# Kernel optimization log

Hardware: AMD Instinct MI355X
Metric: run time of the kernel (lower is better)

## Reference

```python
import jax, jax.numpy as jnp
import numpy as np

B, C, L = 4, 256, 4096
H = 8
DK = C // H


def setup_inputs() -> dict:
    key = jax.random.key(0)
    kx, kq, kk, kv, kl = jax.random.split(key, 5)
    scale = 1.0 / np.sqrt(C)
    return {
        "x": jax.random.normal(kx, (B, C, L), dtype=jnp.float32),
        "Wq": jax.random.normal(kq, (C, C), dtype=jnp.float32) * scale,
        "Wk": jax.random.normal(kk, (C, C), dtype=jnp.float32) * scale,
        "Wv": jax.random.normal(kv, (C, C), dtype=jnp.float32) * scale,
        "Wl": jax.random.normal(kl, (C, C), dtype=jnp.float32) * scale,
    }


def reference(x, Wq, Wk, Wv, Wl):
    # Conv1d with kernel_size=1, no bias == channel-mixing matmul per position.
    def proj(W, t):  # W: [C_out, C_in], t: [B, C_in, L] -> [B, L, H, DK]
        y = jnp.einsum('oc,bcl->blo', W, t)
        return y.reshape(B, L, H, DK)

    q = proj(Wq, x)  # [B, L, H, DK]
    k = proj(Wk, x)
    v = proj(Wv, x)

    # scores: [B, H, L, L]
    scores = jnp.einsum('bqhd,bkhd->bhqk', q, k) / jnp.sqrt(jnp.float32(DK))
    p_attn = jax.nn.softmax(scores, axis=-1)
    # attention output with post-ReLU: [B, L, H, DK] -> [B, L, C]
    out = jax.nn.relu(jnp.einsum('bhqk,bkhd->bqhd', p_attn, v)).reshape(B, L, C)
    # last_conv: [B, C_out, L]
    return jnp.einsum('oc,blc->bol', Wl, out)
```

## Files before the change

kernel.cpp:

```cpp
#include <hip/hip_runtime.h>

#define L_DIM 4096
#define C_DIM 256
#define B_DIM 4
#define NH 8
#define DK 32

#define QSCALE 0.25507694f

typedef __bf16 bf16x8 __attribute__((ext_vector_type(8)));
typedef float  f32x4  __attribute__((ext_vector_type(4)));
typedef float  f32x8  __attribute__((ext_vector_type(8)));
typedef float  f32x16 __attribute__((ext_vector_type(16)));

static __device__ __forceinline__ unsigned pk_bf16(float lo, float hi) {
    unsigned a = __builtin_bit_cast(unsigned, lo) + 0x8000u;
    unsigned b = __builtin_bit_cast(unsigned, hi) + 0x8000u;
    return __builtin_amdgcn_perm(b, a, 0x07060302u);
}

__global__ __launch_bounds__(256) void transpose_x_kernel(
    const float* __restrict__ x, __bf16* __restrict__ xt)
{
    const int t  = threadIdx.x;
    const int l0 = blockIdx.x * 64;
    const int c0 = blockIdx.y * 64;
    const int b  = blockIdx.z;

    __shared__ __attribute__((aligned(16))) float T[64][65];

    {
        const int r  = t >> 2;
        const int lc = (t & 3) * 16;
        const float* xp = x + ((size_t)b * C_DIM + c0 + r) * L_DIM + l0 + lc;
        #pragma unroll
        for (int k = 0; k < 4; ++k)
            *(f32x4*)&T[r][lc + k * 4] = *(const f32x4*)(xp + k * 4);
    }
    __syncthreads();
    {
        const int l  = t >> 2;
        const int cc = (t & 3) * 16;
        unsigned u[8];
        #pragma unroll
        for (int i = 0; i < 8; ++i)
            u[i] = pk_bf16(T[cc + 2 * i][l], T[cc + 2 * i + 1][l]);
        __bf16* op = xt + ((size_t)b * L_DIM + l0 + l) * C_DIM + c0 + cc;
        *(uint4*)op       = make_uint4(u[0], u[1], u[2], u[3]);
        *(uint4*)(op + 8) = make_uint4(u[4], u[5], u[6], u[7]);
    }
}

__global__ __launch_bounds__(256) void proj_mfma_kernel(
    const __bf16* __restrict__ xt, const float* __restrict__ Wq,
    const float* __restrict__ Wk, const float* __restrict__ Wv,
    __bf16* __restrict__ Qb, __bf16* __restrict__ Kb, __bf16* __restrict__ Vb)
{
    const int t    = threadIdx.x;
    const int wave = t >> 6;
    const int lane = t & 63;
    const int n32  = lane & 31;
    const int hl   = lane >> 5;
    const int l0   = blockIdx.x * 128;
    const int ob   = blockIdx.y & 1;
    const int p    = blockIdx.y >> 1;
    const int b    = blockIdx.z;
    const float* W = (p == 0) ? Wq : ((p == 1) ? Wk : Wv);
    const float sc = (p == 0) ? QSCALE : 1.0f;

    __shared__ __attribute__((aligned(16))) __bf16 Wt[128][72];
    __shared__ __attribute__((aligned(16))) __bf16 Xs[128][72];

    const int wo  = t >> 1, wcc = (t & 1) * 32;
    const int xl  = t >> 1, xcc = (t & 1) * 32;
    const float*  wg = W + (size_t)(ob * 128 + wo) * C_DIM + wcc;
    const __bf16* xg = xt + ((size_t)b * L_DIM + l0 + xl) * C_DIM + xcc;

    const int moff = (wave & 1) * 64;
    const int noff = (wave >> 1) * 64;

    f32x16 acc[2][2];
    #pragma unroll
    for (int i = 0; i < 2; ++i)
        #pragma unroll
        for (int j = 0; j < 2; ++j)
            #pragma unroll
            for (int r = 0; r < 16; ++r) acc[i][j][r] = 0.f;

    unsigned wpk[16];
    bf16x8   xpr[4];
    #pragma unroll
    for (int k = 0; k < 8; ++k) {
        f32x4 wv = *(const f32x4*)(wg + k * 4);
        wpk[k * 2]     = pk_bf16(wv[0] * sc, wv[1] * sc);
        wpk[k * 2 + 1] = pk_bf16(wv[2] * sc, wv[3] * sc);
    }
    #pragma unroll
    for (int g = 0; g < 4; ++g) xpr[g] = *(const bf16x8*)(xg + g * 8);

    for (int bk = 0; bk < 4; ++bk) {
        __syncthreads();
        #pragma unroll
        for (int g = 0; g < 4; ++g) {
            *(uint4*)&Wt[wo][wcc + g * 8] =
                make_uint4(wpk[g*4], wpk[g*4+1], wpk[g*4+2], wpk[g*4+3]);
            *(bf16x8*)&Xs[xl][xcc + g * 8] = xpr[g];
        }
        if (bk < 3) {
            #pragma unroll
            for (int k = 0; k < 8; ++k) {
                f32x4 wv = *(const f32x4*)(wg + (bk + 1) * 64 + k * 4);
                wpk[k * 2]     = pk_bf16(wv[0] * sc, wv[1] * sc);
                wpk[k * 2 + 1] = pk_bf16(wv[2] * sc, wv[3] * sc);
            }
            #pragma unroll
            for (int g = 0; g < 4; ++g)
                xpr[g] = *(const bf16x8*)(xg + (bk + 1) * 64 + g * 8);
        }
        __syncthreads();

        #pragma unroll
        for (int ks = 0; ks < 4; ++ks) {
            bf16x8 a0 = *(const bf16x8*)&Wt[moff + n32     ][ks * 16 + hl * 8];
            bf16x8 a1 = *(const bf16x8*)&Wt[moff + 32 + n32][ks * 16 + hl * 8];
            bf16x8 b0 = *(const bf16x8*)&Xs[noff + n32     ][ks * 16 + hl * 8];
            bf16x8 b1 = *(const bf16x8*)&Xs[noff + 32 + n32][ks * 16 + hl * 8];
            acc[0][0] = __builtin_amdgcn_mfma_f32_32x32x16_bf16(a0, b0, acc[0][0], 0, 0, 0);
            acc[0][1] = __builtin_amdgcn_mfma_f32_32x32x16_bf16(a0, b1, acc[0][1], 0, 0, 0);
            acc[1][0] = __builtin_amdgcn_mfma_f32_32x32x16_bf16(a1, b0, acc[1][0], 0, 0, 0);
            acc[1][1] = __builtin_amdgcn_mfma_f32_32x32x16_bf16(a1, b1, acc[1][1], 0, 0, 0);
        }
    }

    #pragma unroll
    for (int mt = 0; mt < 2; ++mt) {
        const int o32 = ob * 128 + moff + mt * 32;
        const int h   = o32 >> 5;
        const int bh  = b * NH + h;
        #pragma unroll
        for (int nt = 0; nt < 2; ++nt) {
            const int l = l0 + noff + nt * 32 + n32;
            if (p < 2) {
                __bf16* out = ((p == 0) ? Qb : Kb) + ((size_t)bh * L_DIM + l) * DK;
                #pragma unroll
                for (int g = 0; g < 4; ++g) {
                    unsigned u0 = pk_bf16(acc[mt][nt][g*4],     acc[mt][nt][g*4+1]);
                    unsigned u1 = pk_bf16(acc[mt][nt][g*4+2],   acc[mt][nt][g*4+3]);
                    *(uint2*)(out + 4 * hl + 8 * g) = make_uint2(u0, u1);
                }
            } else {
                #pragma unroll
                for (int r = 0; r < 16; ++r) {
                    const int dk = (r & 3) + 4 * hl + 8 * (r >> 2);
                    Vb[((size_t)bh * DK + dk) * L_DIM + l] = (__bf16)acc[mt][nt][r];
                }
            }
        }
    }
}

#define SCORE_TILE(K0, K1, V0, V1)                                            \
    _Pragma("unroll")                                                         \
    for (int qt = 0; qt < 2; ++qt) {                                          \
        f32x16 s = __builtin_amdgcn_mfma_f32_32x32x16_bf16(                   \
            K0, qf[qt][0], z16, 0, 0, 0);                                     \
        s = __builtin_amdgcn_mfma_f32_32x32x16_bf16(K1, qf[qt][1], s, 0, 0, 0); \
        f32x8 e0, e1;                                                         \
        _Pragma("unroll")                                                     \
        for (int r = 0; r < 8; ++r) {                                         \
            e0[r] = __builtin_amdgcn_exp2f(s[r]);                             \
            e1[r] = __builtin_amdgcn_exp2f(s[8 + r]);                         \
        }                                                                     \
        bf16x8 p0 = __builtin_convertvector(e0, bf16x8);                      \
        bf16x8 p1 = __builtin_convertvector(e1, bf16x8);                      \
        oacc[qt] = __builtin_amdgcn_mfma_f32_32x32x16_bf16(                   \
            V0, p0, oacc[qt], 0, 0, 0);                                       \
        lacc[qt] = __builtin_amdgcn_mfma_f32_32x32x16_bf16(                   \
            ones, p0, lacc[qt], 0, 0, 0);                                     \
        oacc[qt] = __builtin_amdgcn_mfma_f32_32x32x16_bf16(                   \
            V1, p1, oacc[qt], 0, 0, 0);                                       \
        lacc[qt] = __builtin_amdgcn_mfma_f32_32x32x16_bf16(                   \
            ones, p1, lacc[qt], 0, 0, 0);                                     \
    }

__global__ __launch_bounds__(256) void attn_kernel(
    const __bf16* __restrict__ Q, const __bf16* __restrict__ K,
    const __bf16* __restrict__ V, __bf16* __restrict__ Op0,
    __bf16* __restrict__ Op1, float* __restrict__ Ls)
{
    const int tid   = threadIdx.x;
    const int lane  = tid & 63;
    const int n32   = lane & 31;
    const int hl    = lane >> 5;
    const int wave  = tid >> 6;
    const int h     = blockIdx.y;
    const int b     = blockIdx.z >> 1;
    const int khalf = blockIdx.z & 1;
    const int bh    = b * NH + h;
    const int q0    = blockIdx.x * 256 + wave * 64;

    __shared__ __attribute__((aligned(16))) __bf16 Ks[2][128][40];
    __shared__ __attribute__((aligned(16))) __bf16 Vs[2][32][136];

    bf16x8 qf[2][2];
    #pragma unroll
    for (int qt = 0; qt < 2; ++qt) {
        const __bf16* qp = Q + ((size_t)bh * L_DIM + q0 + qt * 32 + n32) * DK;
        qf[qt][0] = *(const bf16x8*)(qp + hl * 8);
        qf[qt][1] = *(const bf16x8*)(qp + 16 + hl * 8);
    }

    f32x16 oacc[2], lacc[2];
    #pragma unroll
    for (int qt = 0; qt < 2; ++qt)
        #pragma unroll
        for (int r = 0; r < 16; ++r) { oacc[qt][r] = 0.f; lacc[qt][r] = 0.f; }

    const f32x16 z16 = {};

    bf16x8 ones;
    #pragma unroll
    for (int j = 0; j < 8; ++j) ones[j] = (__bf16)1.0f;

    const __bf16* kg = K + (size_t)bh * L_DIM * DK + (size_t)khalf * 2048 * DK
                         + (tid >> 1) * DK + (tid & 1) * 16;
    const __bf16* vg = V + ((size_t)bh * DK + (tid >> 3)) * L_DIM
                         + khalf * 2048 + (tid & 7) * 16;
    const int kr = tid >> 1, kc = (tid & 1) * 16;
    const int j16 = (tid & 7) * 16;
    const int vr  = tid >> 3;

    bf16x8 kreg0 = *(const bf16x8*)(kg);
    bf16x8 kreg1 = *(const bf16x8*)(kg + 8);
    bf16x8 vreg0 = *(const bf16x8*)(vg);
    bf16x8 vreg1 = *(const bf16x8*)(vg + 8);
    {
        *(bf16x8*)&Ks[0][kr][kc]     = kreg0;
        *(bf16x8*)&Ks[0][kr][kc + 8] = kreg1;
        union { bf16x8 v; uint2 u2[2]; } v0, v1;
        v0.v = vreg0; v1.v = vreg1;
        *(uint2*)&Vs[0][vr][j16]      = v0.u2[0];
        *(uint2*)&Vs[0][vr][j16 + 8]  = v0.u2[1];
        *(uint2*)&Vs[0][vr][j16 + 4]  = v1.u2[0];
        *(uint2*)&Vs[0][vr][j16 + 12] = v1.u2[1];
    }
    kreg0 = *(const bf16x8*)(kg + (size_t)1 * 128 * DK);
    kreg1 = *(const bf16x8*)(kg + (size_t)1 * 128 * DK + 8);
    vreg0 = *(const bf16x8*)(vg + 128);
    vreg1 = *(const bf16x8*)(vg + 128 + 8);

    #pragma unroll 2
    for (int kt = 0; kt < 16; ++kt) {
        const int cur = kt & 1;
        __syncthreads();

        bf16x8 kA0 = *(const bf16x8*)&Ks[cur][n32     ][hl * 8];
        bf16x8 kA1 = *(const bf16x8*)&Ks[cur][n32     ][16 + hl * 8];
        bf16x8 kB0 = *(const bf16x8*)&Ks[cur][32 + n32][hl * 8];
        bf16x8 kB1 = *(const bf16x8*)&Ks[cur][32 + n32][16 + hl * 8];
        bf16x8 vA0 = *(const bf16x8*)&Vs[cur][n32][     hl * 8];
        bf16x8 vA1 = *(const bf16x8*)&Vs[cur][n32][16 + hl * 8];
        bf16x8 vB0 = *(const bf16x8*)&Vs[cur][n32][32 + hl * 8];
        bf16x8 vB1 = *(const bf16x8*)&Vs[cur][n32][48 + hl * 8];

        __builtin_amdgcn_s_setprio(1);
        SCORE_TILE(kA0, kA1, vA0, vA1)
        SCORE_TILE(kB0, kB1, vB0, vB1)
        __builtin_amdgcn_s_setprio(0);

        kA0 = *(const bf16x8*)&Ks[cur][64 + n32][hl * 8];
        kA1 = *(const bf16x8*)&Ks[cur][64 + n32][16 + hl * 8];
        kB0 = *(const bf16x8*)&Ks[cur][96 + n32][hl * 8];
        kB1 = *(const bf16x8*)&Ks[cur][96 + n32][16 + hl * 8];
        vA0 = *(const bf16x8*)&Vs[cur][n32][64 + hl * 8];
        vA1 = *(const bf16x8*)&Vs[cur][n32][80 + hl * 8];
        vB0 = *(const bf16x8*)&Vs[cur][n32][96 + hl * 8];
        vB1 = *(const bf16x8*)&Vs[cur][n32][112 + hl * 8];

        if (kt < 15) {
            *(bf16x8*)&Ks[cur ^ 1][kr][kc]     = kreg0;
            *(bf16x8*)&Ks[cur ^ 1][kr][kc + 8] = kreg1;
            union { bf16x8 v; uint2 u2[2]; } v0, v1;
            v0.v = vreg0; v1.v = vreg1;
            *(uint2*)&Vs[cur ^ 1][vr][j16]      = v0.u2[0];
            *(uint2*)&Vs[cur ^ 1][vr][j16 + 8]  = v0.u2[1];
            *(uint2*)&Vs[cur ^ 1][vr][j16 + 4]  = v1.u2[0];
            *(uint2*)&Vs[cur ^ 1][vr][j16 + 12] = v1.u2[1];
            const int nkt = (kt + 2) & 15;
            kreg0 = *(const bf16x8*)(kg + (size_t)nkt * 128 * DK);
            kreg1 = *(const bf16x8*)(kg + (size_t)nkt * 128 * DK + 8);
            vreg0 = *(const bf16x8*)(vg + nkt * 128);
            vreg1 = *(const bf16x8*)(vg + nkt * 128 + 8);
        }

        __builtin_amdgcn_s_setprio(1);
        SCORE_TILE(kA0, kA1, vA0, vA1)
        SCORE_TILE(kB0, kB1, vB0, vB1)
        __builtin_amdgcn_s_setprio(0);
    }

    __bf16* Op = khalf ? Op1 : Op0;
    #pragma unroll
    for (int qt = 0; qt < 2; ++qt) {
        const int l = q0 + qt * 32 + n32;
        __bf16* ap = Op + ((size_t)b * L_DIM + l) * C_DIM + h * 32 + 4 * hl;
        #pragma unroll
        for (int g = 0; g < 4; ++g) {
            *(uint2*)(ap + 8 * g) = make_uint2(
                pk_bf16(oacc[qt][g*4],     oacc[qt][g*4+1]),
                pk_bf16(oacc[qt][g*4+2],   oacc[qt][g*4+3]));
        }
        Ls[((size_t)khalf * B_DIM * NH + bh) * L_DIM + l] = lacc[qt][0];
    }
}

__global__ __launch_bounds__(256) void final_mfma_kernel(
    const __bf16* __restrict__ Op0, const __bf16* __restrict__ Op1,
    const float* __restrict__ Ls, const float* __restrict__ Wl,
    float* __restrict__ y)
{
    const int t    = threadIdx.x;
    const int wave = t >> 6;
    const int lane = t & 63;
    const int n32  = lane & 31;
    const int hl   = lane >> 5;
    const int l0   = blockIdx.x * 64;
    const int ob   = blockIdx.y;
    const int b    = blockIdx.z;

    __shared__ __attribute__((aligned(16))) __bf16 Wt[128][72];
    __shared__ __attribute__((aligned(16))) __bf16 Xs[64][72];

    const int wo  = t >> 1, wcc = (t & 1) * 32;
    const int xl  = t >> 2, xcc = (t & 3) * 16;
    const float* wg = Wl + (size_t)(ob * 128 + wo) * C_DIM + wcc;
    const size_t obase = ((size_t)b * L_DIM + l0 + xl) * C_DIM + xcc;

    float inv[4];
    {
        const int lidx = l0 + xl;
        #pragma unroll
        for (int bk = 0; bk < 4; ++bk) {
            const int hh = (bk * 64 + xcc) >> 5;
            const float l1 = Ls[((size_t)0 * B_DIM * NH + b * NH + hh) * L_DIM + lidx];
            const float l2 = Ls[((size_t)1 * B_DIM * NH + b * NH + hh) * L_DIM + lidx];
            inv[bk] = __builtin_amdgcn_rcpf(l1 + l2);
        }
    }

    const int moff = (wave & 1) * 64;
    const int noff = (wave >> 1) * 32;

    f32x16 acc[2];
    #pragma unroll
    for (int i = 0; i < 2; ++i)
        #pragma unroll
        for (int r = 0; r < 16; ++r) acc[i][r] = 0.f;

    unsigned wpk[16];
    bf16x8   o1r, o2r;
    #pragma unroll
    for (int k = 0; k < 8; ++k) {
        f32x4 wv = *(const f32x4*)(wg + k * 4);
        wpk[k * 2]     = pk_bf16(wv[0], wv[1]);
        wpk[k * 2 + 1] = pk_bf16(wv[2], wv[3]);
    }
    o1r = *(const bf16x8*)(Op0 + obase);
    o2r = *(const bf16x8*)(Op1 + obase);
    bf16x8 o1r2 = *(const bf16x8*)(Op0 + obase + 8);
    bf16x8 o2r2 = *(const bf16x8*)(Op1 + obase + 8);

    for (int bk = 0; bk < 4; ++bk) {
        __syncthreads();
        #pragma unroll
        for (int g = 0; g < 4; ++g)
            *(uint4*)&Wt[wo][wcc + g * 8] =
                make_uint4(wpk[g*4], wpk[g*4+1], wpk[g*4+2], wpk[g*4+3]);
        {
            unsigned u[4];
            #pragma unroll
            for (int i = 0; i < 4; ++i) {
                float v0 = ((float)o1r[2*i]   + (float)o2r[2*i]  ) * inv[bk];
                float v1 = ((float)o1r[2*i+1] + (float)o2r[2*i+1]) * inv[bk];
                v0 = v0 > 0.f ? v0 : 0.f;
                v1 = v1 > 0.f ? v1 : 0.f;
                u[i] = pk_bf16(v0, v1);
            }
            *(uint4*)&Xs[xl][xcc] = make_uint4(u[0], u[1], u[2], u[3]);
            #pragma unroll
            for (int i = 0; i < 4; ++i) {
                float v0 = ((float)o1r2[2*i]   + (float)o2r2[2*i]  ) * inv[bk];
                float v1 = ((float)o1r2[2*i+1] + (float)o2r2[2*i+1]) * inv[bk];
                v0 = v0 > 0.f ? v0 : 0.f;
                v1 = v1 > 0.f ? v1 : 0.f;
                u[i] = pk_bf16(v0, v1);
            }
            *(uint4*)&Xs[xl][xcc + 8] = make_uint4(u[0], u[1], u[2], u[3]);
        }
        if (bk < 3) {
            #pragma unroll
            for (int k = 0; k < 8; ++k) {
                f32x4 wv = *(const f32x4*)(wg + (bk + 1) * 64 + k * 4);
                wpk[k * 2]     = pk_bf16(wv[0], wv[1]);
                wpk[k * 2 + 1] = pk_bf16(wv[2], wv[3]);
            }
            o1r  = *(const bf16x8*)(Op0 + obase + (bk + 1) * 64);
            o2r  = *(const bf16x8*)(Op1 + obase + (bk + 1) * 64);
            o1r2 = *(const bf16x8*)(Op0 + obase + (bk + 1) * 64 + 8);
            o2r2 = *(const bf16x8*)(Op1 + obase + (bk + 1) * 64 + 8);
        }
        __syncthreads();

        #pragma unroll
        for (int ks = 0; ks < 4; ++ks) {
            bf16x8 a0 = *(const bf16x8*)&Wt[moff + n32     ][ks * 16 + hl * 8];
            bf16x8 a1 = *(const bf16x8*)&Wt[moff + 32 + n32][ks * 16 + hl * 8];
            bf16x8 b0 = *(const bf16x8*)&Xs[noff + n32     ][ks * 16 + hl * 8];
            acc[0] = __builtin_amdgcn_mfma_f32_32x32x16_bf16(a0, b0, acc[0], 0, 0, 0);
            acc[1] = __builtin_amdgcn_mfma_f32_32x32x16_bf16(a1, b0, acc[1], 0, 0, 0);
        }
    }

    #pragma unroll
    for (int mt = 0; mt < 2; ++mt) {
        #pragma unroll
        for (int r = 0; r < 16; ++r) {
            const int o = ob * 128 + moff + mt * 32 + (r & 3) + 4 * hl + 8 * (r >> 2);
            y[((size_t)b * C_DIM + o) * L_DIM + l0 + noff + n32] = acc[mt][r];
        }
    }
}

extern "C" void kernel_launch(void* const* d_in, const int* in_sizes, int n_in,
                              void* d_out, int out_size, void* d_ws, size_t ws_size,
                              hipStream_t stream)
{
    const float* x  = (const float*)d_in[0];
    const float* Wq = (const float*)d_in[1];
    const float* Wk = (const float*)d_in[2];
    const float* Wv = (const float*)d_in[3];
    const float* Wl = (const float*)d_in[4];
    float* y = (float*)d_out;

    const size_t n = (size_t)B_DIM * NH * L_DIM * DK;
    __bf16* Qb  = (__bf16*)d_ws;
    __bf16* Kb  = Qb + n;
    __bf16* Vb  = Kb + n;
    __bf16* Xt  = Vb + n;
    __bf16* Op0 = Xt;
    __bf16* Op1 = Xt + n;
    float*  Ls  = (float*)(Op1 + n);

    transpose_x_kernel<<<dim3(L_DIM/64, C_DIM/64, B_DIM), 256, 0, stream>>>(x, Xt);
    proj_mfma_kernel<<<dim3(L_DIM/128, 6, B_DIM), 256, 0, stream>>>(
        Xt, Wq, Wk, Wv, Qb, Kb, Vb);
    attn_kernel<<<dim3(L_DIM/256, NH, B_DIM * 2), 256, 0, stream>>>(
        Qb, Kb, Vb, Op0, Op1, Ls);
    final_mfma_kernel<<<dim3(L_DIM/64, 2, B_DIM), 256, 0, stream>>>(
        Op0, Op1, Ls, Wl, y);
}
```

Measured before the change: 206.2 us.

## Fuse x transpose and bf16 conversion into projection kernel staging

Removes the separate transpose kernel and has the projection kernel read fp32 x directly in [C,L] layout. Each thread converts four channel rows to bf16 and writes them transposed into a swizzled LDS tile, with matching XOR swizzle on the MFMA B-operand reads. This saves one launch plus the write and re-read of the bf16 transposed copy. In exchange, x is now read and converted six times, once per projection/output-block grid slice, and the LDS stores are narrower 8-byte writes.

```diff
diff --git a/kernel.cpp b/kernel.cpp
--- a/kernel.cpp
+++ b/kernel.cpp
@@ -19,40 +19,8 @@
     return __builtin_amdgcn_perm(b, a, 0x07060302u);
 }
 
-__global__ __launch_bounds__(256) void transpose_x_kernel(
-    const float* __restrict__ x, __bf16* __restrict__ xt)
-{
-    const int t  = threadIdx.x;
-    const int l0 = blockIdx.x * 64;
-    const int c0 = blockIdx.y * 64;
-    const int b  = blockIdx.z;
-
-    __shared__ __attribute__((aligned(16))) float T[64][65];
-
-    {
-        const int r  = t >> 2;
-        const int lc = (t & 3) * 16;
-        const float* xp = x + ((size_t)b * C_DIM + c0 + r) * L_DIM + l0 + lc;
-        #pragma unroll
-        for (int k = 0; k < 4; ++k)
-            *(f32x4*)&T[r][lc + k * 4] = *(const f32x4*)(xp + k * 4);
-    }
-    __syncthreads();
-    {
-        const int l  = t >> 2;
-        const int cc = (t & 3) * 16;
-        unsigned u[8];
-        #pragma unroll
-        for (int i = 0; i < 8; ++i)
-            u[i] = pk_bf16(T[cc + 2 * i][l], T[cc + 2 * i + 1][l]);
-        __bf16* op = xt + ((size_t)b * L_DIM + l0 + l) * C_DIM + c0 + cc;
-        *(uint4*)op       = make_uint4(u[0], u[1], u[2], u[3]);
-        *(uint4*)(op + 8) = make_uint4(u[4], u[5], u[6], u[7]);
-    }
-}
-
 __global__ __launch_bounds__(256) void proj_mfma_kernel(
-    const __bf16* __restrict__ xt, const float* __restrict__ Wq,
+    const float* __restrict__ x, const float* __restrict__ Wq,
     const float* __restrict__ Wk, const float* __restrict__ Wv,
     __bf16* __restrict__ Qb, __bf16* __restrict__ Kb, __bf16* __restrict__ Vb)
 {
@@ -72,12 +40,17 @@
     __shared__ __attribute__((aligned(16))) __bf16 Xs[128][72];
 
     const int wo  = t >> 1, wcc = (t & 1) * 32;
-    const int xl  = t >> 1, xcc = (t & 1) * 32;
-    const float*  wg = W + (size_t)(ob * 128 + wo) * C_DIM + wcc;
-    const __bf16* xg = xt + ((size_t)b * L_DIM + l0 + xl) * C_DIM + xcc;
+    const float* wg = W + (size_t)(ob * 128 + wo) * C_DIM + wcc;
+
+    const int lq  = t & 15;
+    const int cg  = t >> 4;
+    const int swW = (lq & 7) * 8;
+    const float* xg = x + ((size_t)b * C_DIM + cg * 4) * L_DIM + l0 + lq * 8;
 
     const int moff = (wave & 1) * 64;
     const int noff = (wave >> 1) * 64;
+    const int sw0  = ((n32 >> 3) & 7) * 8;
+    const int sw1  = ((4 + (n32 >> 3)) & 7) * 8;
 
     f32x16 acc[2][2];
     #pragma unroll
@@ -88,24 +61,38 @@
             for (int r = 0; r < 16; ++r) acc[i][j][r] = 0.f;
 
     unsigned wpk[16];
-    bf16x8   xpr[4];
+    unsigned ux[16];
+
+#define XSTAGE_LOAD(bkk)                                                      \
+    {                                                                         \
+        const float* xp = xg + (size_t)(bkk) * 64 * L_DIM;                    \
+        f32x8 r0 = *(const f32x8*)(xp);                                       \
+        f32x8 r1 = *(const f32x8*)(xp + L_DIM);                               \
+        _Pragma("unroll")                                                     \
+        for (int j = 0; j < 8; ++j) ux[j] = pk_bf16(r0[j], r1[j]);            \
+        f32x8 r2 = *(const f32x8*)(xp + 2 * L_DIM);                           \
+        f32x8 r3 = *(const f32x8*)(xp + 3 * L_DIM);                           \
+        _Pragma("unroll")                                                     \
+        for (int j = 0; j < 8; ++j) ux[8 + j] = pk_bf16(r2[j], r3[j]);        \
+    }
+
     #pragma unroll
     for (int k = 0; k < 8; ++k) {
         f32x4 wv = *(const f32x4*)(wg + k * 4);
         wpk[k * 2]     = pk_bf16(wv[0] * sc, wv[1] * sc);
         wpk[k * 2 + 1] = pk_bf16(wv[2] * sc, wv[3] * sc);
     }
-    #pragma unroll
-    for (int g = 0; g < 4; ++g) xpr[g] = *(const bf16x8*)(xg + g * 8);
+    XSTAGE_LOAD(0)
 
     for (int bk = 0; bk < 4; ++bk) {
         __syncthreads();
         #pragma unroll
-        for (int g = 0; g < 4; ++g) {
+        for (int g = 0; g < 4; ++g)
             *(uint4*)&Wt[wo][wcc + g * 8] =
                 make_uint4(wpk[g*4], wpk[g*4+1], wpk[g*4+2], wpk[g*4+3]);
-            *(bf16x8*)&Xs[xl][xcc + g * 8] = xpr[g];
-        }
+        #pragma unroll
+        for (int j = 0; j < 8; ++j)
+            *(uint2*)&Xs[lq * 8 + j][(cg * 4) ^ swW] = make_uint2(ux[j], ux[8 + j]);
         if (bk < 3) {
             #pragma unroll
             for (int k = 0; k < 8; ++k) {
@@ -113,9 +100,7 @@
                 wpk[k * 2]     = pk_bf16(wv[0] * sc, wv[1] * sc);
                 wpk[k * 2 + 1] = pk_bf16(wv[2] * sc, wv[3] * sc);
             }
-            #pragma unroll
-            for (int g = 0; g < 4; ++g)
-                xpr[g] = *(const bf16x8*)(xg + (bk + 1) * 64 + g * 8);
+            XSTAGE_LOAD(bk + 1)
         }
         __syncthreads();
 
@@ -123,14 +108,15 @@
         for (int ks = 0; ks < 4; ++ks) {
             bf16x8 a0 = *(const bf16x8*)&Wt[moff + n32     ][ks * 16 + hl * 8];
             bf16x8 a1 = *(const bf16x8*)&Wt[moff + 32 + n32][ks * 16 + hl * 8];
-            bf16x8 b0 = *(const bf16x8*)&Xs[noff + n32     ][ks * 16 + hl * 8];
-            bf16x8 b1 = *(const bf16x8*)&Xs[noff + 32 + n32][ks * 16 + hl * 8];
+            bf16x8 b0 = *(const bf16x8*)&Xs[noff + n32     ][(ks * 16 + hl * 8) ^ sw0];
+            bf16x8 b1 = *(const bf16x8*)&Xs[noff + 32 + n32][(ks * 16 + hl * 8) ^ sw1];
             acc[0][0] = __builtin_amdgcn_mfma_f32_32x32x16_bf16(a0, b0, acc[0][0], 0, 0, 0);
             acc[0][1] = __builtin_amdgcn_mfma_f32_32x32x16_bf16(a0, b1, acc[0][1], 0, 0, 0);
             acc[1][0] = __builtin_amdgcn_mfma_f32_32x32x16_bf16(a1, b0, acc[1][0], 0, 0, 0);
             acc[1][1] = __builtin_amdgcn_mfma_f32_32x32x16_bf16(a1, b1, acc[1][1], 0, 0, 0);
         }
     }
+#undef XSTAGE_LOAD
 
     #pragma unroll
     for (int mt = 0; mt < 2; ++mt) {
@@ -446,14 +432,12 @@
     __bf16* Qb  = (__bf16*)d_ws;
     __bf16* Kb  = Qb + n;
     __bf16* Vb  = Kb + n;
-    __bf16* Xt  = Vb + n;
-    __bf16* Op0 = Xt;
-    __bf16* Op1 = Xt + n;
+    __bf16* Op0 = Vb + n;
+    __bf16* Op1 = Op0 + n;
     float*  Ls  = (float*)(Op1 + n);
 
-    transpose_x_kernel<<<dim3(L_DIM/64, C_DIM/64, B_DIM), 256, 0, stream>>>(x, Xt);
     proj_mfma_kernel<<<dim3(L_DIM/128, 6, B_DIM), 256, 0, stream>>>(
-        Xt, Wq, Wk, Wv, Qb, Kb, Vb);
+        x, Wq, Wk, Wv, Qb, Kb, Vb);
     attn_kernel<<<dim3(L_DIM/256, NH, B_DIM * 2), 256, 0, stream>>>(
         Qb, Kb, Vb, Op0, Op1, Ls);
     final_mfma_kernel<<<dim3(L_DIM/64, 2, B_DIM), 256, 0, stream>>>(
```

New measurement: 205.9 us. No clear change (-0.1%).
